# Kernel tuning notes

Measured on AMD Instinct MI355X. Metric: run time of the kernel, lower is better.

## Reference

```python
import jax, jax.numpy as jnp
import numpy as np

NPOINT = 1024
RADIUS = 1.0
NSAMPLE = 32
IN_CH = 64
COOR = 3


def _fps(xyz, npoint):
    # xyz: (B, N, 3) -> (B, npoint) farthest-point-sample indices.
    # Deterministic start at index 0 (torch version starts at a random index;
    # the algorithm/math is otherwise identical).
    B, N, _ = xyz.shape

    def step(carry, _):
        distance, farthest = carry
        centroid = jnp.take_along_axis(xyz, farthest[:, None, None], axis=1)  # (B,1,3)
        d = jnp.sum((xyz - centroid) ** 2, axis=-1)  # squared dist, (B,N)
        distance = jnp.minimum(distance, d)
        nxt = jnp.argmax(distance, axis=-1)
        return (distance, nxt), farthest

    init = (jnp.full((B, N), 1e10, dtype=xyz.dtype), jnp.zeros((B,), dtype=jnp.int32))
    _, idxs = jax.lax.scan(step, init, None, length=npoint)  # (npoint, B)
    return idxs.T  # (B, npoint)


def _sqdist(src, dst):
    # (B,M,C),(B,N,C) -> (B,M,N) squared distances
    return (jnp.sum(src ** 2, -1)[:, :, None]
            - 2.0 * jnp.einsum('bmc,bnc->bmn', src, dst)
            + jnp.sum(dst ** 2, -1)[:, None, :])


def _gather(points, idx):
    # points: (B,N,C); idx: (B,S) or (B,S,G)
    if idx.ndim == 2:
        return jnp.take_along_axis(points, idx[:, :, None], axis=1)
    return jax.vmap(lambda p, i: p[i])(points, idx)


def setup_inputs() -> dict:
    key = jax.random.key(0)
    k1, k2, k3 = jax.random.split(key, 3)
    B, N = 16, 8192
    points_coor = jax.random.normal(k1, (B, COOR, N), dtype=jnp.float32)
    points_fea = jax.random.normal(k2, (B, IN_CH, N), dtype=jnp.float32)
    # Conv2d(in_channel+coor_dim -> 2*in_channel, 1x1, bias=False) weight
    W = jax.random.normal(k3, (2 * IN_CH, IN_CH + COOR), dtype=jnp.float32) * 0.05
    return {"points_coor": points_coor, "points_fea": points_fea, "W": W}


def reference(points_coor, points_fea, W):
    xyz = jnp.transpose(points_coor, (0, 2, 1))  # (B,N,3)
    fea = jnp.transpose(points_fea, (0, 2, 1))   # (B,N,C)
    B, N, _ = xyz.shape

    # S: farthest point sampling
    fps_idx = _fps(xyz, NPOINT)          # (B,S)
    new_coor = _gather(xyz, fps_idx)     # (B,S,3)

    # G: hybrid KNN / ball query
    d = _sqdist(new_coor, xyz)                       # (B,S,N)
    neg_d, group_idx = jax.lax.top_k(-d, NSAMPLE)    # smallest distances
    dvals = -neg_d                                   # (B,S,G)
    group_idx = jnp.where(dvals > RADIUS ** 2, group_idx[:, :, :1], group_idx)

    grouped_coor = _gather(xyz, group_idx)                       # (B,S,G,3)
    grouped_coor = (grouped_coor - new_coor[:, :, None, :]) / RADIUS
    grouped_fea = _gather(fea, group_idx)                        # (B,S,G,C)
    grouped = jnp.concatenate([grouped_fea, grouped_coor], axis=-1)  # (B,S,G,C+3)

    # P: 1x1 conv (no bias, no norm — build_mlp never appends the norm) + ReLU + max-pool over group
    h = jax.nn.relu(jnp.einsum('bsgc,oc->bsgo', grouped, W))     # (B,S,G,2C)
    new_fea = jnp.max(h, axis=2)                                 # (B,S,2C)

    return (jnp.transpose(new_coor, (0, 2, 1)),    # (B,3,S)
            jnp.transpose(new_fea, (0, 2, 1)))     # (B,2C,S)
```

## Files before the change

### kernel.cpp

```cpp
#include <hip/hip_runtime.h>
#include <hip/hip_bf16.h>

#define BB 16
#define NN 8192
#define SS 1024
#define GG 32
#define SORT_R2 0xBF800000u

typedef float v2f __attribute__((ext_vector_type(2)));

__device__ __forceinline__ unsigned sortable(float f) {
    unsigned u = __float_as_uint(f);
    return u ^ ((unsigned)(((int)u) >> 31) | 0x80000000u);
}

template <int CTRL, int RM>
__device__ __forceinline__ float dpp_maxf(float v) {
    int i = __float_as_int(v);
    int p = __builtin_amdgcn_update_dpp(i, i, CTRL, RM, 0xF, false);
    return fmaxf(v, __int_as_float(p));
}

template <int CTRL, int RM>
__device__ __forceinline__ unsigned dpp_minu(unsigned v) {
    int p = __builtin_amdgcn_update_dpp((int)v, (int)v, CTRL, RM, 0xF, false);
    return min(v, (unsigned)p);
}

__device__ __forceinline__ float fmax3(float a, float b, float c) {
    return fmaxf(fmaxf(a, b), c);
}

__global__ __launch_bounds__(256) void k_pts(const float* __restrict__ coor,
                                             float4* __restrict__ pts4) {
    int i = blockIdx.x * 256 + threadIdx.x;
    int b = i >> 13, n = i & (NN - 1);
    const float* cb = coor + (long)b * 3 * NN;
    float x = cb[n], y = cb[NN + n], z = cb[2 * NN + n];
    float pn = __fadd_rn(__fadd_rn(__fmul_rn(x, x), __fmul_rn(y, y)), __fmul_rn(z, z));
    pts4[i] = make_float4(x, y, z, pn);
}

__global__ __launch_bounds__(256) void k_tr(const float* __restrict__ fea,
                                            float* __restrict__ feaT) {
    __shared__ float tile[64][65];
    int b = blockIdx.y, n0 = blockIdx.x * 64;
    int t = threadIdx.x;
    int nl = t & 63, cb = t >> 6;
#pragma unroll
    for (int i = 0; i < 16; i++) {
        int c = cb * 16 + i;
        tile[nl][c] = fea[((long)b * 64 + c) * NN + n0 + nl];
    }
    __syncthreads();
    int cl = t & 63, nb = t >> 6;
#pragma unroll
    for (int i = 0; i < 16; i++) {
        int n = nb * 16 + i;
        feaT[((long)b * NN + n0 + n) * 64 + cl] = tile[n][cl];
    }
}

__global__ __launch_bounds__(512) void k_fps(const float4* __restrict__ pts4,
                                             float4* __restrict__ qpts,
                                             float* __restrict__ out) {
#pragma clang fp contract(off)
    __shared__ float xs[NN], ys[NN], zs[NN];
    __shared__ int scur[SS];
    __shared__ __align__(16) float redv[2][8];
    __shared__ int sidx[2];
    int b = blockIdx.x;
    int t = threadIdx.x;
    const float4* P = pts4 + (long)b * NN;

    v2f px[8], py[8], pz[8], dist[8];
#pragma unroll
    for (int j = 0; j < 8; j++) {
        int p0 = t + (2 * j) * 512;
        int p1 = t + (2 * j + 1) * 512;
        float4 a = P[p0];
        float4 c = P[p1];
        px[j] = v2f{a.x, c.x};
        py[j] = v2f{a.y, c.y};
        pz[j] = v2f{a.z, c.z};
        dist[j] = v2f{1e10f, 1e10f};
        xs[p0] = a.x; ys[p0] = a.y; zs[p0] = a.z;
        xs[p1] = c.x; ys[p1] = c.y; zs[p1] = c.z;
    }
    if (t == 0) { sidx[0] = 0x7FFFFFFF; sidx[1] = 0x7FFFFFFF; }
    __syncthreads();

    int cur = 0;
    for (int s = 0; s < SS; s++) {
        int par = s & 1;
        float cx = xs[cur], cy = ys[cur], cz = zs[cur];
        if (t == 0) scur[s] = cur;
        v2f cx2 = v2f{cx, cx}, cy2 = v2f{cy, cy}, cz2 = v2f{cz, cz};
#pragma unroll
        for (int j = 0; j < 8; j++) {
            v2f dx = px[j] - cx2;
            v2f dy = py[j] - cy2;
            v2f dz = pz[j] - cz2;
            v2f xx = dx * dx;
            v2f yy = dy * dy;
            v2f zz = dz * dz;
            v2f sm = xx + yy;
            v2f d = sm + zz;
            dist[j] = __builtin_elementwise_min(dist[j], d);
        }
        v2f m01 = __builtin_elementwise_max(dist[0], dist[1]);
        v2f m23 = __builtin_elementwise_max(dist[2], dist[3]);
        v2f m45 = __builtin_elementwise_max(dist[4], dist[5]);
        v2f m67 = __builtin_elementwise_max(dist[6], dist[7]);
        v2f m03 = __builtin_elementwise_max(m01, m23);
        v2f m47 = __builtin_elementwise_max(m45, m67);
        v2f m07 = __builtin_elementwise_max(m03, m47);
        float bv = fmaxf(m07.x, m07.y);
        float wv = bv;
        wv = dpp_maxf<0x111, 0xF>(wv);
        wv = dpp_maxf<0x112, 0xF>(wv);
        wv = dpp_maxf<0x114, 0xF>(wv);
        wv = dpp_maxf<0x118, 0xF>(wv);
        wv = dpp_maxf<0x142, 0xA>(wv);
        wv = dpp_maxf<0x143, 0xC>(wv);
        if ((t & 63) == 63) redv[par][t >> 6] = wv;
        __syncthreads();
        float4 r0 = *(const float4*)redv[par];
        float4 r1 = *(const float4*)(redv[par] + 4);
        float gmax = fmaxf(fmax3(r0.x, r0.y, r0.z),
                           fmax3(r0.w, fmax3(r1.x, r1.y, r1.z), r1.w));
        if (t == 0) sidx[1 - par] = 0x7FFFFFFF;
        if (bv == gmax) {
            int jj = 16;
#pragma unroll
            for (int j = 7; j >= 0; j--) {
                jj = (dist[j].y == gmax) ? (2 * j + 1) : jj;
                jj = (dist[j].x == gmax) ? (2 * j) : jj;
            }
            atomicMin(&sidx[par], t + jj * 512);
        }
        __syncthreads();
        cur = sidx[par];
    }
    __syncthreads();

#pragma unroll
    for (int s = t; s < SS; s += 512) {
        int c = scur[s];
        float cx = xs[c], cy = ys[c], cz = zs[c];
        out[(long)b * 3 * SS + s]          = cx;
        out[(long)b * 3 * SS + SS + s]     = cy;
        out[(long)b * 3 * SS + 2 * SS + s] = cz;
        float qn = __fadd_rn(__fadd_rn(__fmul_rn(cx, cx), __fmul_rn(cy, cy)),
                             __fmul_rn(cz, cz));
        qpts[(long)b * SS + s] = make_float4(cx, cy, cz, qn);
    }
}

#define SKEW(p) ((p) + ((p) >> 5))
__global__ __launch_bounds__(64, 1) void k_knn_mlp(const float4* __restrict__ pts4,
                                                   const float* __restrict__ feaT,
                                                   const float4* __restrict__ qpts,
                                                   const float* __restrict__ W,
                                                   float* __restrict__ out) {
    __shared__ __align__(16) unsigned dk[NN + NN / 32];
    __shared__ int sidxs[GG];
    float* grouped = (float*)dk;

    int Q = blockIdx.x;
    int b = Q >> 10, s = Q & 1023;
    int l = threadIdx.x;
    float4 q = qpts[Q];
    const float4* P = pts4 + (long)b * NN;

    unsigned bmin = 0xFFFFFFFFu;
    int bpos = 0;
#pragma unroll 16
    for (int j = 0; j < 128; j++) {
        int p = j * 64 + l;
        float4 v = P[p];
        float dot = __fadd_rn(__fadd_rn(__fmul_rn(q.x, v.x), __fmul_rn(q.y, v.y)),
                              __fmul_rn(q.z, v.z));
        float d = __fadd_rn(__fsub_rn(q.w, __fmul_rn(2.0f, dot)), v.w);
        unsigned u = sortable(d);
        dk[SKEW(p)] = u;
        if (u < bmin) { bmin = u; bpos = p; }
    }
    __syncthreads();

    float wa[68], wb[68];
    {
        const float* Wr = W + l * 67;
#pragma unroll
        for (int c = 0; c < 67; c++) {
            wa[c] = Wr[c];
            wb[c] = Wr[64 * 67 + c];
        }
        wa[67] = 0.f; wb[67] = 0.f;
    }

    unsigned resv = 0;
    int resp = 0, pos0 = 0;
    for (int k = 0; k < GG; k++) {
        unsigned mv = bmin;
        mv = dpp_minu<0x111, 0xF>(mv);
        mv = dpp_minu<0x112, 0xF>(mv);
        mv = dpp_minu<0x114, 0xF>(mv);
        mv = dpp_minu<0x118, 0xF>(mv);
        mv = dpp_minu<0x142, 0xA>(mv);
        mv = dpp_minu<0x143, 0xC>(mv);
        unsigned wmin = (unsigned)__builtin_amdgcn_readlane((int)mv, 63);
        unsigned long long mask = __ballot(bmin == wmin);
        int wpos;
        if (__builtin_popcountll(mask) == 1) {
            int owner = __builtin_ctzll(mask);
            wpos = __builtin_amdgcn_readlane(bpos, owner);
        } else {
            unsigned long long kk =
                ((unsigned long long)bmin << 32) | (unsigned)bpos;
#pragma unroll
            for (int m = 1; m < 64; m <<= 1) {
                unsigned long long o = __shfl_xor(kk, m, 64);
                kk = (o < kk) ? o : kk;
            }
            wpos = (int)(kk & 0xFFFFFFFFull);
        }
        if (k == 0) pos0 = wpos;
        if (l == k) { resv = wmin; resp = wpos; }
        int own = wpos & 63;
        if (l == own) dk[SKEW(wpos)] = 0xFFFFFFFFu;
        __syncthreads();
        int p1 = l * 64 + own;
        int p2 = (l + 64) * 64 + own;
        unsigned v1 = dk[SKEW(p1)], v2 = dk[SKEW(p2)];
        bool c = v2 < v1;
        unsigned cv = c ? v2 : v1;
        int cp = c ? p2 : p1;
        unsigned cm = cv;
        cm = dpp_minu<0x111, 0xF>(cm);
        cm = dpp_minu<0x112, 0xF>(cm);
        cm = dpp_minu<0x114, 0xF>(cm);
        cm = dpp_minu<0x118, 0xF>(cm);
        cm = dpp_minu<0x142, 0xA>(cm);
        cm = dpp_minu<0x143, 0xC>(cm);
        unsigned colmin = (unsigned)__builtin_amdgcn_readlane((int)cm, 63);
        unsigned long long m2 = __ballot(cv == colmin);
        int colpos;
        if (__builtin_popcountll(m2) == 1) {
            colpos = __builtin_amdgcn_readlane(cp, __builtin_ctzll(m2));
        } else {
            unsigned long long kk =
                ((unsigned long long)cv << 32) | (unsigned)cp;
#pragma unroll
            for (int m = 1; m < 64; m <<= 1) {
                unsigned long long o = __shfl_xor(kk, m, 64);
                kk = (o < kk) ? o : kk;
            }
            colpos = (int)(kk & 0xFFFFFFFFull);
        }
        if (l == own) { bmin = colmin; bpos = colpos; }
        __syncthreads();
    }

    if (l < GG) sidxs[l] = (resv > SORT_R2) ? pos0 : resp;
    __syncthreads();

    if (l < 32) {
        int idx = sidxs[l];
        float4 p = pts4[(long)b * NN + idx];
        float4 rc = make_float4(__fsub_rn(p.x, q.x), __fsub_rn(p.y, q.y),
                                __fsub_rn(p.z, q.z), 0.f);
        *(float4*)&grouped[l * 68 + 64] = rc;
    }
    {
        int g = l >> 1, half = l & 1;
        int idx = sidxs[g];
        const float4* f4 = (const float4*)(feaT + ((long)b * NN + idx) * 64);
#pragma unroll
        for (int k4 = 0; k4 < 8; k4++) {
            *(float4*)&grouped[g * 68 + half * 32 + k4 * 4] = f4[half * 8 + k4];
        }
    }
    __syncthreads();

    float m0 = -1e30f, m1 = -1e30f;
#pragma unroll 2
    for (int g = 0; g < GG; g++) {
        float a0 = 0.f, a1 = 0.f;
#pragma unroll
        for (int c4 = 0; c4 < 17; c4++) {
            float4 gv = *(float4*)&grouped[g * 68 + c4 * 4];
            a0 = fmaf(gv.x, wa[4 * c4 + 0], a0);
            a0 = fmaf(gv.y, wa[4 * c4 + 1], a0);
            a0 = fmaf(gv.z, wa[4 * c4 + 2], a0);
            a0 = fmaf(gv.w, wa[4 * c4 + 3], a0);
            a1 = fmaf(gv.x, wb[4 * c4 + 0], a1);
            a1 = fmaf(gv.y, wb[4 * c4 + 1], a1);
            a1 = fmaf(gv.z, wb[4 * c4 + 2], a1);
            a1 = fmaf(gv.w, wb[4 * c4 + 3], a1);
        }
        m0 = fmaxf(m0, a0);
        m1 = fmaxf(m1, a1);
    }
    out[49152 + ((long)b * 128 + l) * SS + s]      = fmaxf(m0, 0.f);
    out[49152 + ((long)b * 128 + l + 64) * SS + s] = fmaxf(m1, 0.f);
}

extern "C" void kernel_launch(void* const* d_in, const int* in_sizes, int n_in,
                              void* d_out, int out_size, void* d_ws, size_t ws_size,
                              hipStream_t stream) {
    const float* coor = (const float*)d_in[0];
    const float* fea  = (const float*)d_in[1];
    const float* Wm   = (const float*)d_in[2];
    float* out = (float*)d_out;

    char* ws = (char*)d_ws;
    float4* pts4 = (float4*)ws;
    float*  feaT = (float*)(ws + 2097152);
    float4* qpts = (float4*)(ws + 2097152 + 33554432);

    k_pts<<<(BB * NN) / 256, 256, 0, stream>>>(coor, pts4);
    k_tr<<<dim3(NN / 64, BB), 256, 0, stream>>>(fea, feaT);
    k_fps<<<BB, 512, 0, stream>>>(pts4, qpts, out);
    k_knn_mlp<<<BB * SS, 64, 0, stream>>>(pts4, feaT, qpts, Wm, out);
}
```

Before: 1.489 ms.

## Morton-sort points per FPS thread and skip updates via bounding-box lower bound

Computes a per-batch bounding box, assigns each point a 6-bit-per-axis Morton key, and bitonic-sorts all 8192 keys in shared memory. Each thread then owns 16 spatially contiguous points and keeps their bounding box. In each FPS step, a thread skips its distance update when the box's lower-bound distance to the current centroid cannot shrink its running maximum. The argmax tie-break now uses original indices. The cost is an upfront sort with 91 block barriers and more shared memory, in exchange for skipping much of the per-step distance arithmetic. Wavefront divergence may limit how much is actually skipped.

New measurement: 1.633 ms. 1.1x slower.

```diff
diff --git a/kernel.cpp b/kernel.cpp
--- a/kernel.cpp
+++ b/kernel.cpp
@@ -22,6 +22,13 @@
 }
 
 template <int CTRL, int RM>
+__device__ __forceinline__ float dpp_minf(float v) {
+    int i = __float_as_int(v);
+    int p = __builtin_amdgcn_update_dpp(i, i, CTRL, RM, 0xF, false);
+    return fminf(v, __int_as_float(p));
+}
+
+template <int CTRL, int RM>
 __device__ __forceinline__ unsigned dpp_minu(unsigned v) {
     int p = __builtin_amdgcn_update_dpp((int)v, (int)v, CTRL, RM, 0xF, false);
     return min(v, (unsigned)p);
@@ -29,6 +36,13 @@
 
 __device__ __forceinline__ float fmax3(float a, float b, float c) {
     return fmaxf(fmaxf(a, b), c);
+}
+
+__device__ __forceinline__ unsigned spread3(unsigned c) {
+    unsigned r = 0;
+#pragma unroll
+    for (int b = 0; b < 6; b++) r |= ((c >> b) & 1u) << (3 * b);
+    return r;
 }
 
 __global__ __launch_bounds__(256) void k_pts(const float* __restrict__ coor,
@@ -61,33 +75,115 @@
     }
 }
 
-__global__ __launch_bounds__(512) void k_fps(const float4* __restrict__ pts4,
-                                             float4* __restrict__ qpts,
-                                             float* __restrict__ out) {
+__global__ __launch_bounds__(512, 2) void k_fps(const float4* __restrict__ pts4,
+                                                float4* __restrict__ qpts,
+                                                float* __restrict__ out) {
 #pragma clang fp contract(off)
     __shared__ float xs[NN], ys[NN], zs[NN];
     __shared__ int scur[SS];
+    __shared__ unsigned skey[NN];
     __shared__ __align__(16) float redv[2][8];
+    __shared__ float bbred[6][8];
     __shared__ int sidx[2];
     int b = blockIdx.x;
     int t = threadIdx.x;
     const float4* P = pts4 + (long)b * NN;
 
+    float lminx = 1e30f, lmaxx = -1e30f;
+    float lminy = 1e30f, lmaxy = -1e30f;
+    float lminz = 1e30f, lmaxz = -1e30f;
+#pragma unroll
+    for (int j = 0; j < 16; j++) {
+        int p = t + j * 512;
+        float4 v = P[p];
+        xs[p] = v.x; ys[p] = v.y; zs[p] = v.z;
+        lminx = fminf(lminx, v.x); lmaxx = fmaxf(lmaxx, v.x);
+        lminy = fminf(lminy, v.y); lmaxy = fmaxf(lmaxy, v.y);
+        lminz = fminf(lminz, v.z); lmaxz = fmaxf(lmaxz, v.z);
+    }
+    if (t == 0) { sidx[0] = 0x7FFFFFFF; sidx[1] = 0x7FFFFFFF; }
+    lminx = dpp_minf<0x111,0xF>(lminx); lminx = dpp_minf<0x112,0xF>(lminx);
+    lminx = dpp_minf<0x114,0xF>(lminx); lminx = dpp_minf<0x118,0xF>(lminx);
+    lminx = dpp_minf<0x142,0xA>(lminx); lminx = dpp_minf<0x143,0xC>(lminx);
+    lminy = dpp_minf<0x111,0xF>(lminy); lminy = dpp_minf<0x112,0xF>(lminy);
+    lminy = dpp_minf<0x114,0xF>(lminy); lminy = dpp_minf<0x118,0xF>(lminy);
+    lminy = dpp_minf<0x142,0xA>(lminy); lminy = dpp_minf<0x143,0xC>(lminy);
+    lminz = dpp_minf<0x111,0xF>(lminz); lminz = dpp_minf<0x112,0xF>(lminz);
+    lminz = dpp_minf<0x114,0xF>(lminz); lminz = dpp_minf<0x118,0xF>(lminz);
+    lminz = dpp_minf<0x142,0xA>(lminz); lminz = dpp_minf<0x143,0xC>(lminz);
+    lmaxx = dpp_maxf<0x111,0xF>(lmaxx); lmaxx = dpp_maxf<0x112,0xF>(lmaxx);
+    lmaxx = dpp_maxf<0x114,0xF>(lmaxx); lmaxx = dpp_maxf<0x118,0xF>(lmaxx);
+    lmaxx = dpp_maxf<0x142,0xA>(lmaxx); lmaxx = dpp_maxf<0x143,0xC>(lmaxx);
+    lmaxy = dpp_maxf<0x111,0xF>(lmaxy); lmaxy = dpp_maxf<0x112,0xF>(lmaxy);
+    lmaxy = dpp_maxf<0x114,0xF>(lmaxy); lmaxy = dpp_maxf<0x118,0xF>(lmaxy);
+    lmaxy = dpp_maxf<0x142,0xA>(lmaxy); lmaxy = dpp_maxf<0x143,0xC>(lmaxy);
+    lmaxz = dpp_maxf<0x111,0xF>(lmaxz); lmaxz = dpp_maxf<0x112,0xF>(lmaxz);
+    lmaxz = dpp_maxf<0x114,0xF>(lmaxz); lmaxz = dpp_maxf<0x118,0xF>(lmaxz);
+    lmaxz = dpp_maxf<0x142,0xA>(lmaxz); lmaxz = dpp_maxf<0x143,0xC>(lmaxz);
+    if ((t & 63) == 63) {
+        int w = t >> 6;
+        bbred[0][w] = lminx; bbred[1][w] = lmaxx;
+        bbred[2][w] = lminy; bbred[3][w] = lmaxy;
+        bbred[4][w] = lminz; bbred[5][w] = lmaxz;
+    }
+    __syncthreads();
+    float bminx = bbred[0][0], bmaxx = bbred[1][0];
+    float bminy = bbred[2][0], bmaxy = bbred[3][0];
+    float bminz = bbred[4][0], bmaxz = bbred[5][0];
+#pragma unroll
+    for (int w = 1; w < 8; w++) {
+        bminx = fminf(bminx, bbred[0][w]); bmaxx = fmaxf(bmaxx, bbred[1][w]);
+        bminy = fminf(bminy, bbred[2][w]); bmaxy = fmaxf(bmaxy, bbred[3][w]);
+        bminz = fminf(bminz, bbred[4][w]); bmaxz = fmaxf(bmaxz, bbred[5][w]);
+    }
+    float sxs = 63.0f / fmaxf(bmaxx - bminx, 1e-20f);
+    float sys = 63.0f / fmaxf(bmaxy - bminy, 1e-20f);
+    float szs = 63.0f / fmaxf(bmaxz - bminz, 1e-20f);
+#pragma unroll
+    for (int j = 0; j < 16; j++) {
+        int p = t + j * 512;
+        unsigned c0 = (unsigned)(int)fminf(63.f, fmaxf(0.f, (xs[p] - bminx) * sxs));
+        unsigned c1 = (unsigned)(int)fminf(63.f, fmaxf(0.f, (ys[p] - bminy) * sys));
+        unsigned c2 = (unsigned)(int)fminf(63.f, fmaxf(0.f, (zs[p] - bminz) * szs));
+        unsigned mo = spread3(c0) | (spread3(c1) << 1) | (spread3(c2) << 2);
+        skey[p] = (mo << 13) | (unsigned)p;
+    }
+    __syncthreads();
+    for (int kk = 2; kk <= NN; kk <<= 1) {
+        for (int jj = kk >> 1; jj > 0; jj >>= 1) {
+#pragma unroll 1
+            for (int m = 0; m < 16; m++) {
+                int i = m * 512 + t;
+                int ixj = i ^ jj;
+                if (ixj > i) {
+                    unsigned a = skey[i], c = skey[ixj];
+                    bool up = ((i & kk) == 0);
+                    if ((a > c) == up) { skey[i] = c; skey[ixj] = a; }
+                }
+            }
+            __syncthreads();
+        }
+    }
     v2f px[8], py[8], pz[8], dist[8];
-#pragma unroll
-    for (int j = 0; j < 8; j++) {
-        int p0 = t + (2 * j) * 512;
-        int p1 = t + (2 * j + 1) * 512;
-        float4 a = P[p0];
-        float4 c = P[p1];
-        px[j] = v2f{a.x, c.x};
-        py[j] = v2f{a.y, c.y};
-        pz[j] = v2f{a.z, c.z};
-        dist[j] = v2f{1e10f, 1e10f};
-        xs[p0] = a.x; ys[p0] = a.y; zs[p0] = a.z;
-        xs[p1] = c.x; ys[p1] = c.y; zs[p1] = c.z;
-    }
-    if (t == 0) { sidx[0] = 0x7FFFFFFF; sidx[1] = 0x7FFFFFFF; }
+    int oidx[16];
+    float gxmin = 1e30f, gxmax = -1e30f;
+    float gymin = 1e30f, gymax = -1e30f;
+    float gzmin = 1e30f, gzmax = -1e30f;
+#pragma unroll
+    for (int j = 0; j < 16; j++) {
+        int o = (int)(skey[t * 16 + j] & (NN - 1));
+        oidx[j] = o;
+        float x = xs[o], y = ys[o], z = zs[o];
+        gxmin = fminf(gxmin, x); gxmax = fmaxf(gxmax, x);
+        gymin = fminf(gymin, y); gymax = fmaxf(gymax, y);
+        gzmin = fminf(gzmin, z); gzmax = fmaxf(gzmax, z);
+        int pr = j >> 1;
+        if (j & 1) { px[pr].y = x; py[pr].y = y; pz[pr].y = z; }
+        else       { px[pr].x = x; py[pr].x = y; pz[pr].x = z; }
+    }
+#pragma unroll
+    for (int j = 0; j < 8; j++) dist[j] = v2f{1e10f, 1e10f};
+    float bv = 1e10f;
     __syncthreads();
 
     int cur = 0;
@@ -95,27 +191,33 @@
         int par = s & 1;
         float cx = xs[cur], cy = ys[cur], cz = zs[cur];
         if (t == 0) scur[s] = cur;
-        v2f cx2 = v2f{cx, cx}, cy2 = v2f{cy, cy}, cz2 = v2f{cz, cz};
-#pragma unroll
-        for (int j = 0; j < 8; j++) {
-            v2f dx = px[j] - cx2;
-            v2f dy = py[j] - cy2;
-            v2f dz = pz[j] - cz2;
-            v2f xx = dx * dx;
-            v2f yy = dy * dy;
-            v2f zz = dz * dz;
-            v2f sm = xx + yy;
-            v2f d = sm + zz;
-            dist[j] = __builtin_elementwise_min(dist[j], d);
-        }
-        v2f m01 = __builtin_elementwise_max(dist[0], dist[1]);
-        v2f m23 = __builtin_elementwise_max(dist[2], dist[3]);
-        v2f m45 = __builtin_elementwise_max(dist[4], dist[5]);
-        v2f m67 = __builtin_elementwise_max(dist[6], dist[7]);
-        v2f m03 = __builtin_elementwise_max(m01, m23);
-        v2f m47 = __builtin_elementwise_max(m45, m67);
-        v2f m07 = __builtin_elementwise_max(m03, m47);
-        float bv = fmaxf(m07.x, m07.y);
+        float ax = fmax3(gxmin - cx, cx - gxmax, 0.0f);
+        float ay = fmax3(gymin - cy, cy - gymax, 0.0f);
+        float az = fmax3(gzmin - cz, cz - gzmax, 0.0f);
+        float lb = (ax * ax + ay * ay) + az * az;
+        if (lb * 0.9999847412109375f < bv) {
+            v2f cx2 = v2f{cx, cx}, cy2 = v2f{cy, cy}, cz2 = v2f{cz, cz};
+#pragma unroll
+            for (int j = 0; j < 8; j++) {
+                v2f dx = px[j] - cx2;
+                v2f dy = py[j] - cy2;
+                v2f dz = pz[j] - cz2;
+                v2f xx = dx * dx;
+                v2f yy = dy * dy;
+                v2f zz = dz * dz;
+                v2f sm = xx + yy;
+                v2f d = sm + zz;
+                dist[j] = __builtin_elementwise_min(dist[j], d);
+            }
+            v2f m01 = __builtin_elementwise_max(dist[0], dist[1]);
+            v2f m23 = __builtin_elementwise_max(dist[2], dist[3]);
+            v2f m45 = __builtin_elementwise_max(dist[4], dist[5]);
+            v2f m67 = __builtin_elementwise_max(dist[6], dist[7]);
+            v2f m03 = __builtin_elementwise_max(m01, m23);
+            v2f m47 = __builtin_elementwise_max(m45, m67);
+            v2f m07 = __builtin_elementwise_max(m03, m47);
+            bv = fmaxf(m07.x, m07.y);
+        }
         float wv = bv;
         wv = dpp_maxf<0x111, 0xF>(wv);
         wv = dpp_maxf<0x112, 0xF>(wv);
@@ -131,13 +233,13 @@
                            fmax3(r0.w, fmax3(r1.x, r1.y, r1.z), r1.w));
         if (t == 0) sidx[1 - par] = 0x7FFFFFFF;
         if (bv == gmax) {
-            int jj = 16;
-#pragma unroll
-            for (int j = 7; j >= 0; j--) {
-                jj = (dist[j].y == gmax) ? (2 * j + 1) : jj;
-                jj = (dist[j].x == gmax) ? (2 * j) : jj;
+            int mi = 0x7FFFFFFF;
+#pragma unroll
+            for (int j = 0; j < 8; j++) {
+                mi = min(mi, (dist[j].x == gmax) ? oidx[2 * j]     : 0x7FFFFFFF);
+                mi = min(mi, (dist[j].y == gmax) ? oidx[2 * j + 1] : 0x7FFFFFFF);
             }
-            atomicMin(&sidx[par], t + jj * 512);
+            atomicMin(&sidx[par], mi);
         }
         __syncthreads();
         cur = sidx[par];
```
